# Kernel optimization log

Hardware: AMD Instinct MI355X
Metric: run time of the kernel (lower is better)

The kernel has to match this reference:

```python
import jax, jax.numpy as jnp
import numpy as np

B, C, H, W = 512, 3, 64, 32
K = 2                      # fractional pool kernel size
HOUT, WOUT = 38, 16        # floor(64*0.6), floor(32*0.5)
HID = 128                  # RNN hidden size
D = C * HOUT               # RNN input size = 114


def _frac_starts(in_size, out_size, k, u=0.5):
    # PyTorch fractional-max-pool interval formula with deterministic sample u
    alpha = (in_size - k) / (out_size - 1)
    i = np.arange(out_size - 1)
    starts = np.floor((i + u) * alpha) - np.floor(u * alpha)
    return np.concatenate([starts, [in_size - k]]).astype(np.int32)

ROW = _frac_starts(H, HOUT, K)   # (HOUT,) window start rows
COL = _frac_starts(W, WOUT, K)   # (WOUT,) window start cols


def setup_inputs() -> dict:
    key = jax.random.key(0)
    ks = jax.random.split(key, 5)
    s = 1.0 / np.sqrt(HID)  # torch RNNCell init scale
    return {
        "x": jax.random.normal(ks[0], (B, C, H, W), jnp.float32),
        "W_ih": jax.random.uniform(ks[1], (HID, D), jnp.float32, -s, s),
        "W_hh": jax.random.uniform(ks[2], (HID, HID), jnp.float32, -s, s),
        "b_ih": jax.random.uniform(ks[3], (HID,), jnp.float32, -s, s),
        "b_hh": jax.random.uniform(ks[4], (HID,), jnp.float32, -s, s),
    }


def reference(x, W_ih, W_hh, b_ih, b_hh):
    # 1) fractional max pool, kernel 2: pairwise max over gathered window starts
    xr = jnp.maximum(x[:, :, ROW, :], x[:, :, ROW + 1, :])          # (B,C,HOUT,W)
    pooled = jnp.maximum(xr[:, :, :, COL], xr[:, :, :, COL + 1])    # (B,C,HOUT,WOUT)
    # 2) exact (erf-based) GELU, matching torch nn.GELU default
    act = jax.nn.gelu(pooled, approximate=False)
    # 3) sequence over width: (WOUT, B, C*HOUT), C-major flatten matches torch view
    seq = act.transpose(3, 0, 1, 2).reshape(WOUT, B, D)
    # 4) vanilla RNNCell across time via scan
    def step(h, xt):
        h = jnp.tanh(xt @ W_ih.T + b_ih + h @ W_hh.T + b_hh)
        return h, h
    _, outs = jax.lax.scan(step, jnp.zeros((B, HID), x.dtype), seq)  # (WOUT,B,HID)
    # 5) temporal mean + tanh
    t_mean = jnp.tanh(outs.mean(axis=0))                             # (B,HID)
    # 6) modulate by global spatial mean of pooled; torch broadcasting of
    #    (B,HID) * (B,1,1,1) yields (B,1,B,HID) — replicated faithfully
    s_mean = pooled.mean(axis=(1, 2, 3), keepdims=True)              # (B,1,1,1)
    return t_mean * s_mean                                           # (B,1,B,HID)
```

## Files before the change

### kernel.cpp

```cpp
#include <hip/hip_runtime.h>
#include <math.h>

#define BB   512
#define CC   3
#define HH   64
#define WW   32
#define HOUT 38
#define WOUT 16
#define HID  128
#define DD   114
#define SEQP 120
#define WIHP 120
#define WHHP 132
#define NPOOL (CC*HOUT*WOUT)

typedef float f32x4 __attribute__((ext_vector_type(4)));

__device__ __forceinline__ float fast_tanh(float u) {
    return 1.f - 2.f / (__expf(2.f * u) + 1.f);
}

#define WS_SMEAN 0
#define WS_TMEAN 512

__global__ __launch_bounds__(256, 2)
void k1_fused(const float* __restrict__ x,
              const float* __restrict__ Wih,
              const float* __restrict__ Whh,
              const float* __restrict__ bih,
              const float* __restrict__ bhh,
              float* __restrict__ s_mean,
              float* __restrict__ t_mean)
{
    __shared__ __align__(16) float wst[HID * WIHP];
    __shared__ __align__(16) float seq[WOUT][SEQP];
    __shared__ __align__(16) float Zl[WOUT][HID];
    __shared__ __align__(16) float hbuf[2][HID];
    __shared__ float psum[HID];
    __shared__ float red[4];
    __shared__ int   rowl[HOUT];

    const int tid  = threadIdx.x;
    const int half = tid >> 7;
    const int k    = tid & 127;
    const int wid  = tid >> 6;
    const int lane = tid & 63;
    const int b    = blockIdx.x;

    f32x4 xpf[6];
    {
        const f32x4* xg = (const f32x4*)(x + (size_t)b * (CC*HH*WW));
        #pragma unroll
        for (int i = 0; i < 6; ++i) xpf[i] = xg[tid + 256*i];
    }
    f32x4 wihpf[14], wihtail;
    {
        const f32x4* wg = (const f32x4*)Wih;
        #pragma unroll
        for (int i = 0; i < 14; ++i) wihpf[i] = wg[tid + 256*i];
        if (tid < 64) wihtail = wg[3584 + tid];
    }

    if (tid < HOUT) {
        double alpha = (double)(HH - 2) / (double)(HOUT - 1);
        rowl[tid] = (tid < HOUT - 1)
            ? (int)(floor((tid + 0.5) * alpha) - floor(0.5 * alpha))
            : (HH - 2);
    }
    if (tid < HID) hbuf[0][tid] = 0.f;
    if (tid < 96)  seq[tid / 6][DD + tid % 6] = 0.f;

    {
        f32x4* xd = (f32x4*)wst;
        #pragma unroll
        for (int i = 0; i < 6; ++i) xd[tid + 256*i] = xpf[i];
    }
    __syncthreads();

    float ps = 0.f;
    #pragma unroll
    for (int it = 0; it < 8; ++it) {
        int idx = tid + it*256;
        if (idx < NPOOL) {
            int c  = idx / (HOUT*WOUT);
            int r  = idx % (HOUT*WOUT);
            int ho = r / WOUT;
            int wo = r % WOUT;
            const float* p0 = &wst[c*(HH*WW) + rowl[ho]*WW + 2*wo];
            float m = fmaxf(fmaxf(p0[0], p0[1]), fmaxf(p0[WW], p0[WW+1]));
            ps += m;
            seq[wo][c*HOUT + ho] =
                0.5f * m * (1.f + erff(m * 0.70710678118654752440f));
        }
    }
    #pragma unroll
    for (int off = 32; off > 0; off >>= 1) ps += __shfl_down(ps, off);
    if (lane == 0) red[wid] = ps;
    __syncthreads();
    if (tid == 0)
        s_mean[b] = (red[0] + red[1] + red[2] + red[3]) * (1.f / (float)NPOOL);

    #pragma unroll
    for (int i = 0; i < 14; ++i) {
        int j = 4*(tid + 256*i);
        #pragma unroll
        for (int e = 0; e < 4; ++e) {
            int r  = (j + e) / DD;
            int cc = (j + e) - r*DD;
            wst[r*WIHP + cc] = wihpf[i][e];
        }
    }
    if (tid < 64) {
        int j = 4*(3584 + tid);
        #pragma unroll
        for (int e = 0; e < 4; ++e) {
            int r  = (j + e) / DD;
            int cc = (j + e) - r*DD;
            wst[r*WIHP + cc] = wihtail[e];
        }
    }
    for (int j = tid; j < HID*6; j += 256)
        wst[(j/6)*WIHP + DD + (j % 6)] = 0.f;
    __syncthreads();

    f32x4 wih[15];
    {
        const f32x4* wr = (const f32x4*)&wst[k*WIHP + half*60];
        #pragma unroll
        for (int dd = 0; dd < 15; ++dd) wih[dd] = wr[dd];
    }

    f32x4 whhpf[8];
    {
        const f32x4* hg = (const f32x4*)Whh;
        #pragma unroll
        for (int i = 0; i < 8; ++i) whhpf[i] = hg[tid + 256*i];
    }

    float zreg[WOUT];
    #pragma unroll
    for (int t = 0; t < WOUT; ++t) {
        const f32x4* a4 = (const f32x4*)&seq[t][half*60];
        float s0 = 0.f, s1 = 0.f, s2 = 0.f, s3 = 0.f;
        #pragma unroll
        for (int dd = 0; dd < 15; ++dd) {
            f32x4 a = a4[dd];
            s0 = fmaf(wih[dd].x, a.x, s0);
            s1 = fmaf(wih[dd].y, a.y, s1);
            s2 = fmaf(wih[dd].z, a.z, s2);
            s3 = fmaf(wih[dd].w, a.w, s3);
        }
        float zp = (s0 + s1) + (s2 + s3);
        if (half) Zl[t][k] = zp; else zreg[t] = zp;
    }
    __syncthreads();
    {
        const float bias = bih[k] + bhh[k];
        if (!half) {
            #pragma unroll
            for (int t = 0; t < WOUT; ++t) zreg[t] += bias + Zl[t][k];
        }
    }

    f32x4 whh[16];
    #pragma unroll
    for (int i = 0; i < 8; ++i) {
        int j4 = tid + 256*i;
        *(f32x4*)&wst[(j4 >> 5)*WHHP + ((j4 & 31) << 2)] = whhpf[i];
    }
    __syncthreads();
    if ((k >> 6) == 0) {
        const f32x4* wr = (const f32x4*)&wst[(k & 63)*WHHP + (half << 6)];
        #pragma unroll
        for (int dd = 0; dd < 16; ++dd) whh[dd] = wr[dd];
    }
    {
        const f32x4* hg = (const f32x4*)(Whh + 64*HID);
        #pragma unroll
        for (int i = 0; i < 8; ++i) whhpf[i] = hg[tid + 256*i];
    }
    __syncthreads();
    #pragma unroll
    for (int i = 0; i < 8; ++i) {
        int j4 = tid + 256*i;
        *(f32x4*)&wst[(j4 >> 5)*WHHP + ((j4 & 31) << 2)] = whhpf[i];
    }
    __syncthreads();
    if ((k >> 6) == 1) {
        const f32x4* wr = (const f32x4*)&wst[(k & 63)*WHHP + (half << 6)];
        #pragma unroll
        for (int dd = 0; dd < 16; ++dd) whh[dd] = wr[dd];
    }

    float hsum = 0.f;
    #pragma unroll
    for (int t = 0; t < WOUT; ++t) {
        const int cur = t & 1, nxt = cur ^ 1;
        const f32x4* h4 = (const f32x4*)&hbuf[cur][half << 6];
        float s0 = 0.f, s1 = 0.f, s2 = 0.f, s3 = 0.f;
        #pragma unroll
        for (int dd = 0; dd < 16; ++dd) {
            f32x4 hv = h4[dd];
            s0 = fmaf(whh[dd].x, hv.x, s0);
            s1 = fmaf(whh[dd].y, hv.y, s1);
            s2 = fmaf(whh[dd].z, hv.z, s2);
            s3 = fmaf(whh[dd].w, hv.w, s3);
        }
        float up = (s0 + s1) + (s2 + s3);
        if (half) psum[k] = up;
        __syncthreads();
        if (!half) {
            float hn = fast_tanh(zreg[t] + up + psum[k]);
            hsum += hn;
            hbuf[nxt][k] = hn;
        }
        __syncthreads();
    }
    if (!half) t_mean[b*HID + k] = fast_tanh(hsum * (1.f / 16.f));
}

__global__ __launch_bounds__(256)
void k2_out(const float* __restrict__ s_mean,
            const float* __restrict__ t_mean,
            f32x4* __restrict__ out)
{
    const int i   = blockIdx.x >> 3;
    const int sub = blockIdx.x & 7;
    const float s = s_mean[i];
    const f32x4* t4 = (const f32x4*)t_mean + sub*2048;
    f32x4*       o  = out + (size_t)i*16384 + sub*2048;
    const int tid = threadIdx.x;
    #pragma unroll
    for (int j = 0; j < 8; ++j) {
        int idx = tid + j*256;
        o[idx] = s * t4[idx];
    }
}

extern "C" void kernel_launch(void* const* d_in, const int* in_sizes, int n_in,
                              void* d_out, int out_size, void* d_ws, size_t ws_size,
                              hipStream_t stream)
{
    const float* x   = (const float*)d_in[0];
    const float* Wih = (const float*)d_in[1];
    const float* Whh = (const float*)d_in[2];
    const float* bih = (const float*)d_in[3];
    const float* bhh = (const float*)d_in[4];

    float* ws     = (float*)d_ws;
    float* s_mean = ws + WS_SMEAN;
    float* t_mean = ws + WS_TMEAN;

    k1_fused<<<dim3(BB), dim3(256), 0, stream>>>(x, Wih, Whh, bih, bhh, s_mean, t_mean);
    k2_out  <<<dim3(4096), dim3(256), 0, stream>>>(s_mean, t_mean, (f32x4*)d_out);
}
```

Measured before the change: 49.82 us.

## Pair hidden-unit halves within a wavefront and combine via shuffle

Remaps threads so the two half-dot-products for each hidden unit sit in lanes 32 apart in the same wavefront, and combines them with a cross-lane xor shuffle instead of shared-memory partial sums. This removes one block barrier per RNN time step and the Zl/psum shared buffers. W_hh is now staged in a single pass, with LDS sized for the padded W_hh layout. The cost is more prefetch registers (16 vectors) and both lanes computing a redundant tanh.

```diff
diff --git a/kernel.cpp b/kernel.cpp
--- a/kernel.cpp
+++ b/kernel.cpp
@@ -32,19 +32,17 @@
               float* __restrict__ s_mean,
               float* __restrict__ t_mean)
 {
-    __shared__ __align__(16) float wst[HID * WIHP];
+    __shared__ __align__(16) float wst[HID * WHHP];
     __shared__ __align__(16) float seq[WOUT][SEQP];
-    __shared__ __align__(16) float Zl[WOUT][HID];
     __shared__ __align__(16) float hbuf[2][HID];
-    __shared__ float psum[HID];
     __shared__ float red[4];
     __shared__ int   rowl[HOUT];
 
     const int tid  = threadIdx.x;
-    const int half = tid >> 7;
-    const int k    = tid & 127;
     const int wid  = tid >> 6;
     const int lane = tid & 63;
+    const int kl   = (wid << 5) | (lane & 31);
+    const int kc   = lane >> 5;
     const int b    = blockIdx.x;
 
     f32x4 xpf[6];
@@ -125,22 +123,22 @@
 
     f32x4 wih[15];
     {
-        const f32x4* wr = (const f32x4*)&wst[k*WIHP + half*60];
+        const f32x4* wr = (const f32x4*)&wst[kl*WIHP + kc*60];
         #pragma unroll
         for (int dd = 0; dd < 15; ++dd) wih[dd] = wr[dd];
     }
 
-    f32x4 whhpf[8];
+    f32x4 whhpf[16];
     {
         const f32x4* hg = (const f32x4*)Whh;
         #pragma unroll
-        for (int i = 0; i < 8; ++i) whhpf[i] = hg[tid + 256*i];
+        for (int i = 0; i < 16; ++i) whhpf[i] = hg[tid + 256*i];
     }
 
     float zreg[WOUT];
     #pragma unroll
     for (int t = 0; t < WOUT; ++t) {
-        const f32x4* a4 = (const f32x4*)&seq[t][half*60];
+        const f32x4* a4 = (const f32x4*)&seq[t][kc*60];
         float s0 = 0.f, s1 = 0.f, s2 = 0.f, s3 = 0.f;
         #pragma unroll
         for (int dd = 0; dd < 15; ++dd) {
@@ -150,44 +148,25 @@
             s2 = fmaf(wih[dd].z, a.z, s2);
             s3 = fmaf(wih[dd].w, a.w, s3);
         }
-        float zp = (s0 + s1) + (s2 + s3);
-        if (half) Zl[t][k] = zp; else zreg[t] = zp;
-    }
-    __syncthreads();
-    {
-        const float bias = bih[k] + bhh[k];
-        if (!half) {
-            #pragma unroll
-            for (int t = 0; t < WOUT; ++t) zreg[t] += bias + Zl[t][k];
-        }
-    }
-
-    f32x4 whh[16];
-    #pragma unroll
-    for (int i = 0; i < 8; ++i) {
+        float p = (s0 + s1) + (s2 + s3);
+        zreg[t] = p + __shfl_xor(p, 32);
+    }
+    {
+        const float bias = bih[kl] + bhh[kl];
+        #pragma unroll
+        for (int t = 0; t < WOUT; ++t) zreg[t] += bias;
+    }
+    __syncthreads();
+
+    #pragma unroll
+    for (int i = 0; i < 16; ++i) {
         int j4 = tid + 256*i;
         *(f32x4*)&wst[(j4 >> 5)*WHHP + ((j4 & 31) << 2)] = whhpf[i];
     }
     __syncthreads();
-    if ((k >> 6) == 0) {
-        const f32x4* wr = (const f32x4*)&wst[(k & 63)*WHHP + (half << 6)];
-        #pragma unroll
-        for (int dd = 0; dd < 16; ++dd) whh[dd] = wr[dd];
-    }
-    {
-        const f32x4* hg = (const f32x4*)(Whh + 64*HID);
-        #pragma unroll
-        for (int i = 0; i < 8; ++i) whhpf[i] = hg[tid + 256*i];
-    }
-    __syncthreads();
-    #pragma unroll
-    for (int i = 0; i < 8; ++i) {
-        int j4 = tid + 256*i;
-        *(f32x4*)&wst[(j4 >> 5)*WHHP + ((j4 & 31) << 2)] = whhpf[i];
-    }
-    __syncthreads();
-    if ((k >> 6) == 1) {
-        const f32x4* wr = (const f32x4*)&wst[(k & 63)*WHHP + (half << 6)];
+    f32x4 whh[16];
+    {
+        const f32x4* wr = (const f32x4*)&wst[kl*WHHP + (kc << 6)];
         #pragma unroll
         for (int dd = 0; dd < 16; ++dd) whh[dd] = wr[dd];
     }
@@ -196,7 +175,7 @@
     #pragma unroll
     for (int t = 0; t < WOUT; ++t) {
         const int cur = t & 1, nxt = cur ^ 1;
-        const f32x4* h4 = (const f32x4*)&hbuf[cur][half << 6];
+        const f32x4* h4 = (const f32x4*)&hbuf[cur][kc << 6];
         float s0 = 0.f, s1 = 0.f, s2 = 0.f, s3 = 0.f;
         #pragma unroll
         for (int dd = 0; dd < 16; ++dd) {
@@ -206,17 +185,14 @@
             s2 = fmaf(whh[dd].z, hv.z, s2);
             s3 = fmaf(whh[dd].w, hv.w, s3);
         }
-        float up = (s0 + s1) + (s2 + s3);
-        if (half) psum[k] = up;
+        float p  = (s0 + s1) + (s2 + s3);
+        float u  = zreg[t] + p + __shfl_xor(p, 32);
+        float hn = fast_tanh(u);
+        hsum += hn;
+        if (kc == 0) hbuf[nxt][kl] = hn;
         __syncthreads();
-        if (!half) {
-            float hn = fast_tanh(zreg[t] + up + psum[k]);
-            hsum += hn;
-            hbuf[nxt][k] = hn;
-        }
-        __syncthreads();
-    }
-    if (!half) t_mean[b*HID + k] = fast_tanh(hsum * (1.f / 16.f));
+    }
+    if (kc == 0) t_mean[b*HID + kl] = fast_tanh(hsum * (1.f / 16.f));
 }
 
 __global__ __launch_bounds__(256)
```

New measurement: 48.46 us. 2.7% less time.
